# Kernel tuning notes

Measured on AMD Instinct MI355X. Metric: run time of the kernel, lower is better.

Reference implementation:

```python
import jax, jax.numpy as jnp
import numpy as np

# ---- static config (matches init_kwargs) ----
B = 8            # batch_size (graphs)
N = 10000        # num_nodes per graph
NTOT = B * N     # total node rows (80000)
E = 320000       # edges (only over first N nodes, as in the original code)
D = 128          # input_dim == backbone_channels (shared conv forces equality)
H = 4            # heads
C = 128          # backbone_channels (per-head out dim, concat=False)
L = 3            # num_backbone_layers
K = 30           # sort-pool k
HID = 512        # mlp_hidden_dim
OUT = 2          # output_dim
EXPECTED = K * L * C * H + 1  # buggy mlp_input_dim from __init__ -> zero-pad
BN_EPS = 1e-5


def setup_inputs() -> dict:
    key = jax.random.key(0)
    ks = jax.random.split(key, 20)
    s = 1.0 / np.sqrt(D)
    inp = {
        "x": jax.random.normal(ks[0], (NTOT, D), dtype=jnp.float32),
        "edge_index": jax.random.randint(ks[1], (2, E), 0, N, dtype=jnp.int32),
        "age": jax.random.normal(ks[2], (B,), dtype=jnp.float32),
        # shared TransformerConv params (reused across all L layers)
        "Wq": jax.random.normal(ks[3], (D, H * C), dtype=jnp.float32) * s,
        "bq": jax.random.normal(ks[4], (H * C,), dtype=jnp.float32) * 0.02,
        "Wk": jax.random.normal(ks[5], (D, H * C), dtype=jnp.float32) * s,
        "bk": jax.random.normal(ks[6], (H * C,), dtype=jnp.float32) * 0.02,
        "Wv": jax.random.normal(ks[7], (D, H * C), dtype=jnp.float32) * s,
        "bv": jax.random.normal(ks[8], (H * C,), dtype=jnp.float32) * 0.02,
        "Wskip": jax.random.normal(ks[9], (D, C), dtype=jnp.float32) * s,
        "bskip": jax.random.normal(ks[10], (C,), dtype=jnp.float32) * 0.02,
        # per-layer BatchNorm (eval mode: running stats)
        "bn_gamma": 1.0 + 0.1 * jax.random.normal(ks[11], (L, C), dtype=jnp.float32),
        "bn_beta": 0.1 * jax.random.normal(ks[12], (L, C), dtype=jnp.float32),
        "bn_mean": 0.1 * jax.random.normal(ks[13], (L, C), dtype=jnp.float32),
        "bn_var": jax.random.uniform(ks[14], (L, C), dtype=jnp.float32, minval=0.5, maxval=1.5),
        # MLP head (2 layers: EXPECTED->HID, ReLU, HID->OUT)
        "W1": jax.random.normal(ks[15], (EXPECTED, HID), dtype=jnp.float32) * (1.0 / np.sqrt(EXPECTED)),
        "b1": jnp.zeros((HID,), dtype=jnp.float32),
        "W2": jax.random.normal(ks[16], (HID, OUT), dtype=jnp.float32) * (1.0 / np.sqrt(HID)),
        "b2": jnp.zeros((OUT,), dtype=jnp.float32),
    }
    return inp


def _transformer_conv(h, src, dst, Wq, bq, Wk, bk, Wv, bv, Wskip, bskip):
    # PyG TransformerConv, concat=False, root_weight=True, eval (no attn dropout)
    q = (h @ Wq + bq).reshape(NTOT, H, C)
    k = (h @ Wk + bk).reshape(NTOT, H, C)
    v = (h @ Wv + bv).reshape(NTOT, H, C)
    # per-edge attention logits [E, H]
    alpha = jnp.einsum("ehc,ehc->eh", q[dst], k[src]) / np.sqrt(C).astype(np.float32)
    # segment softmax over incoming edges of each target node
    m = jax.ops.segment_max(alpha, dst, num_segments=NTOT)          # [NTOT, H]
    e = jnp.exp(alpha - m[dst])
    denom = jax.ops.segment_sum(e, dst, num_segments=NTOT)          # [NTOT, H]
    a = e / (denom[dst] + 1e-16)                                    # [E, H]
    out = jax.ops.segment_sum(a[:, :, None] * v[src], dst, num_segments=NTOT)  # [NTOT,H,C]
    return out.mean(axis=1) + h @ Wskip + bskip                     # concat=False -> head mean


def reference(x, edge_index, age, Wq, bq, Wk, bk, Wv, bv, Wskip, bskip,
              bn_gamma, bn_beta, bn_mean, bn_var, W1, b1, W2, b2):
    src, dst = edge_index[0], edge_index[1]
    h = x
    feats = []
    for i in range(L):  # fixed small layer count; shared conv weights
        h = _transformer_conv(h, src, dst, Wq, bq, Wk, bk, Wv, bv, Wskip, bskip)
        h = (h - bn_mean[i]) * (bn_gamma[i] / jnp.sqrt(bn_var[i] + BN_EPS)) + bn_beta[i]
        h = jax.nn.relu(h)  # dropout: eval mode no-op
        feats.append(h)
    h = feats[-1]  # concat_input_graph=False
    # global_sort_pool: sort nodes per graph by last channel (desc), take top-k
    xr = h.reshape(B, N, C)
    idx = jnp.argsort(-xr[:, :, -1], axis=1)[:, :K]                 # [B, K]
    pooled = jnp.take_along_axis(xr, idx[:, :, None], axis=1)       # [B, K, C]
    z = pooled.reshape(B, K * C)
    z = jnp.concatenate([z, age.reshape(B, 1)], axis=1)             # [B, K*C+1]
    # zero-pad to the (mismatched) expected MLP input dim, as in the original
    z = jnp.concatenate([z, jnp.zeros((B, EXPECTED - z.shape[1]), dtype=z.dtype)], axis=1)
    z = jax.nn.relu(z @ W1 + b1)
    z = z @ W2 + b2
    return jax.nn.log_softmax(z, axis=-1)
```

## Files before the change

kernel.cpp:

```cpp
#include <hip/hip_runtime.h>
#include <cmath>


#define NN    10000
#define NTOT  80000
#define EE    320000
#define CH    128

__device__ __forceinline__ float rl_f(float v, int lane) {
    return __uint_as_float(__builtin_amdgcn_readlane(__float_as_uint(v), lane));
}

__global__ __launch_bounds__(256) void precompute_kernel(
    const float* __restrict__ Wq, const float* __restrict__ bq,
    const float* __restrict__ Wk, const float* __restrict__ Wv,
    const float* __restrict__ bv, const float* __restrict__ Wskip,
    const float* __restrict__ bskip,
    const float* __restrict__ bn_gamma, const float* __restrict__ bn_beta,
    const float* __restrict__ bn_mean, const float* __restrict__ bn_var,
    float* __restrict__ Bcat, float* __restrict__ biascat,
    float* __restrict__ Wcomb, float* __restrict__ bvbar,
    float* __restrict__ bnS, float* __restrict__ bnB)
{
    const float inv_sqrtC = 0.08838834764831845f;
    int idx = blockIdx.x * 256 + threadIdx.x;
    if (idx < 65536) {
        int c = idx >> 9;
        int o = idx & 511;
        int hbase = o & ~127;
        int j = o & 127;
        const float* wq = Wq + c * 512 + hbase;
        const float* wk = Wk + j * 512 + hbase;
        float s = 0.f;
        for (int cc = 0; cc < 128; cc++) s = fmaf(wq[cc], wk[cc], s);
        Bcat[c * 640 + o] = s * inv_sqrtC;
        return;
    }
    idx -= 65536;
    if (idx < 16384) {
        int c = idx >> 7, n = idx & 127;
        Bcat[c * 640 + 512 + n] = Wskip[c * 128 + n];
        return;
    }
    idx -= 16384;
    if (idx < 512) {
        int o = idx, hbase = o & ~127, j = o & 127;
        const float* wk = Wk + j * 512 + hbase;
        const float* bqp = bq + hbase;
        float s = 0.f;
        for (int cc = 0; cc < 128; cc++) s = fmaf(bqp[cc], wk[cc], s);
        biascat[o] = s * inv_sqrtC;
        return;
    }
    idx -= 512;
    if (idx < 128) {
        biascat[512 + idx] = bskip[idx];
        return;
    }
    idx -= 128;
    if (idx < 65536) {
        int k = idx >> 7;
        int n = idx & 127;
        int h = k >> 7, c = k & 127;
        Wcomb[k * 128 + n] = Wv[c * 512 + h * 128 + n] * 0.25f;
        return;
    }
    idx -= 65536;
    if (idx < 128) {
        float s = 0.f;
        for (int h = 0; h < 4; h++) s += bv[h * 128 + idx];
        bvbar[idx] = 0.25f * s;
        return;
    }
    idx -= 128;
    if (idx < 384) {
        float sc = bn_gamma[idx] / sqrtf(bn_var[idx] + 1e-5f);
        bnS[idx] = sc;
        bnB[idx] = bn_beta[idx] - bn_mean[idx] * sc;
        return;
    }
}

__global__ void count_kernel(const int* __restrict__ dst, int* __restrict__ deg) {
    int e = blockIdx.x * 256 + threadIdx.x;
    if (e < EE) atomicAdd(&deg[dst[e]], 1);
}

__global__ __launch_bounds__(1024) void scan_kernel(const int* __restrict__ deg,
                                                    int* __restrict__ rowstart) {
    __shared__ int part[1024];
    const int t = threadIdx.x;
    int loc[10];
    int s = 0;
    for (int i = 0; i < 10; i++) {
        int idx = t * 10 + i;
        int v = (idx < NN) ? deg[idx] : 0;
        loc[i] = s; s += v;
    }
    part[t] = s; __syncthreads();
    for (int d = 1; d < 1024; d <<= 1) {
        int v = (t >= d) ? part[t - d] : 0;
        __syncthreads();
        part[t] += v;
        __syncthreads();
    }
    int base = (t == 0) ? 0 : part[t - 1];
    for (int i = 0; i < 10; i++) {
        int idx = t * 10 + i;
        if (idx <= NN) rowstart[idx] = base + loc[i];
    }
}

__global__ void scatter_kernel(const int* __restrict__ src, const int* __restrict__ dst,
                               const int* __restrict__ rowstart, int* __restrict__ cursor,
                               int* __restrict__ csr_src) {
    int e = blockIdx.x * 256 + threadIdx.x;
    if (e < EE) {
        int d = dst[e];
        int p = atomicAdd(&cursor[d], 1);
        csr_src[rowstart[d] + p] = src[e];
    }
}

__global__ __launch_bounds__(256, 3) void skip_keys_kernel(
    const float* __restrict__ xup,
    const float* __restrict__ Wskip,
    const float* __restrict__ bskip,
    const float* __restrict__ bnS, const float* __restrict__ bnB,
    float* __restrict__ gkeys)
{
    __shared__ float rowb[64][132];
    __shared__ float Bs[16][132];
    __shared__ float sWc[128];
    const int t = threadIdx.x;
    const int r0 = blockIdx.x * 64;
    const int Mrem = min(64, (NTOT - NN) - r0);
    const int tx = t & 15;
    const int ty = t >> 4;

    for (int f = t; f < 64 * 32; f += 256) {
        int row = f >> 5, c4 = (f & 31) * 4;
        if (row < Mrem)
            *(float4*)&rowb[row][c4] = *(const float4*)(xup + (size_t)(r0 + row) * CH + c4);
    }
    if (t < 128) sWc[t] = Wskip[t * 128 + 127];

    for (int l = 0; l < 2; l++) {
        float acc[4][8];
        #pragma unroll
        for (int i = 0; i < 4; i++)
            #pragma unroll
            for (int j = 0; j < 8; j++) acc[i][j] = 0.f;

        for (int k0 = 0; k0 < 128; k0 += 16) {
            __syncthreads();
            for (int f = t; f < 512; f += 256) {
                int kk = f >> 5, n4 = (f & 31) * 4;
                *(float4*)&Bs[kk][n4] = *(const float4*)(Wskip + (size_t)(k0 + kk) * 128 + n4);
            }
            __syncthreads();
            #pragma unroll
            for (int kq = 0; kq < 4; kq++) {
                float4 a4[4];
                #pragma unroll
                for (int i = 0; i < 4; i++)
                    a4[i] = *(const float4*)&rowb[ty + 16 * i][k0 + kq * 4];
                float4 c0[4], c1[4];
                #pragma unroll
                for (int q = 0; q < 4; q++) {
                    c0[q] = *(const float4*)&Bs[kq * 4 + q][tx * 4];
                    c1[q] = *(const float4*)&Bs[kq * 4 + q][64 + tx * 4];
                }
                #pragma unroll
                for (int q = 0; q < 4; q++) {
                    #pragma unroll
                    for (int i = 0; i < 4; i++) {
                        const float av = (q == 0) ? a4[i].x : (q == 1) ? a4[i].y
                                       : (q == 2) ? a4[i].z : a4[i].w;
                        acc[i][0] = fmaf(av, c0[q].x, acc[i][0]);
                        acc[i][1] = fmaf(av, c0[q].y, acc[i][1]);
                        acc[i][2] = fmaf(av, c0[q].z, acc[i][2]);
                        acc[i][3] = fmaf(av, c0[q].w, acc[i][3]);
                        acc[i][4] = fmaf(av, c1[q].x, acc[i][4]);
                        acc[i][5] = fmaf(av, c1[q].y, acc[i][5]);
                        acc[i][6] = fmaf(av, c1[q].z, acc[i][6]);
                        acc[i][7] = fmaf(av, c1[q].w, acc[i][7]);
                    }
                }
            }
        }
        __syncthreads();
        const float* bS = bnS + l * 128;
        const float* bB = bnB + l * 128;
        #pragma unroll
        for (int i = 0; i < 4; i++) {
            const int row = ty + 16 * i;
            float4 v0, v1;
            float* p0 = &v0.x;
            float* p1 = &v1.x;
            #pragma unroll
            for (int q = 0; q < 4; q++) {
                const int n0c = tx * 4 + q;
                float xv = acc[i][q] + bskip[n0c];
                xv = fmaf(xv, bS[n0c], bB[n0c]);
                p0[q] = fmaxf(xv, 0.f);
                const int n1c = 64 + tx * 4 + q;
                float yv = acc[i][4 + q] + bskip[n1c];
                yv = fmaf(yv, bS[n1c], bB[n1c]);
                p1[q] = fmaxf(yv, 0.f);
            }
            *(float4*)&rowb[row][tx * 4] = v0;
            *(float4*)&rowb[row][64 + tx * 4] = v1;
        }
    }
    __syncthreads();
    if (t < Mrem) {
        float s = 0.f;
        for (int k = 0; k < 128; k++) s = fmaf(rowb[t][k], sWc[k], s);
        s += bskip[127];
        s = fmaf(s, bnS[2 * 128 + 127], bnB[2 * 128 + 127]);
        gkeys[NN + r0 + t] = fmaxf(s, 0.f);
    }
}

template<int BM, int BN, int TM, int TN, int MODE>
__global__ __launch_bounds__(256) void gemm_fp32(
    const float* __restrict__ A, int lda,
    const float* __restrict__ B, int ldb,
    const float* __restrict__ bias, const float* __restrict__ bias2,
    const int* __restrict__ deg,
    const float* __restrict__ Cold,
    const float* __restrict__ bnS, const float* __restrict__ bnB,
    float* __restrict__ C0, int ldc0,
    float* __restrict__ C1, int ldc1,
    int M, int K,
    float* __restrict__ keysOut)
{
    constexpr int BK = 16;
    __shared__ float As[BK][BM + 4];
    __shared__ float Bs[BK][BN + 4];
    const int t  = threadIdx.x;
    const int tx = t % (BN / TN);
    const int ty = t / (BN / TN);
    const int m0 = blockIdx.x * BM;
    const int n0 = blockIdx.y * BN;
    float acc[TM][TN];
    #pragma unroll
    for (int i = 0; i < TM; i++)
        #pragma unroll
        for (int j = 0; j < TN; j++) acc[i][j] = 0.f;

    for (int k0 = 0; k0 < K; k0 += BK) {
        #pragma unroll
        for (int f = t; f < BM * 4; f += 256) {
            int row = f >> 2, fc = f & 3;
            int gm = m0 + row;
            float4 v = make_float4(0.f, 0.f, 0.f, 0.f);
            if (gm < M) v = *(const float4*)(A + (size_t)gm * lda + k0 + fc * 4);
            As[fc * 4 + 0][row] = v.x;
            As[fc * 4 + 1][row] = v.y;
            As[fc * 4 + 2][row] = v.z;
            As[fc * 4 + 3][row] = v.w;
        }
        #pragma unroll
        for (int f = t; f < BK * (BN / 4); f += 256) {
            int kk = f / (BN / 4);
            int nn = (f % (BN / 4)) * 4;
            *(float4*)(&Bs[kk][nn]) = *(const float4*)(B + (size_t)(k0 + kk) * ldb + n0 + nn);
        }
        __syncthreads();
        #pragma unroll
        for (int kk = 0; kk < BK; kk++) {
            float af[TM], bf[TN];
            if constexpr (TM == 2) {
                float2 v = *(const float2*)&As[kk][ty * 2];
                af[0] = v.x; af[1] = v.y;
            } else {
                float4 v = *(const float4*)&As[kk][ty * 4];
                af[0] = v.x; af[1] = v.y; af[2] = v.z; af[3] = v.w;
            }
            if constexpr (TN == 4) {
                float4 v = *(const float4*)&Bs[kk][tx * 4];
                bf[0] = v.x; bf[1] = v.y; bf[2] = v.z; bf[3] = v.w;
            } else {
                float4 v = *(const float4*)&Bs[kk][tx * 4];
                float4 w = *(const float4*)&Bs[kk][BN / 2 + tx * 4];
                bf[0] = v.x; bf[1] = v.y; bf[2] = v.z; bf[3] = v.w;
                bf[4] = w.x; bf[5] = w.y; bf[6] = w.z; bf[7] = w.w;
            }
            #pragma unroll
            for (int i = 0; i < TM; i++)
                #pragma unroll
                for (int j = 0; j < TN; j++)
                    acc[i][j] = fmaf(af[i], bf[j], acc[i][j]);
        }
        __syncthreads();
    }
    #pragma unroll
    for (int i = 0; i < TM; i++) {
        const int gm = m0 + ty * TM + i;
        if (gm >= M) continue;
        const bool addB2 = (MODE == 4) ? (deg[gm] > 0) : false;
        #pragma unroll
        for (int h = 0; h < TN / 4; h++) {
            const int nb = n0 + ((TN == 8) ? h * (BN / 2) + tx * 4 : tx * TN + h * 4);
            float4 v;
            float* vp = &v.x;
            if (MODE == 4) {
                const float4 old = *(const float4*)(Cold + (size_t)gm * ldc1 + nb);
                const float* op = &old.x;
                #pragma unroll
                for (int q = 0; q < 4; q++) {
                    const int n = nb + q;
                    float x = acc[i][h * 4 + q] + op[q];
                    if (addB2) x += bias2[n];
                    x = fmaf(x, bnS[n], bnB[n]);
                    vp[q] = fmaxf(x, 0.f);
                }
                *(float4*)(C0 + (size_t)gm * ldc0 + nb) = v;
                if (keysOut != nullptr && nb == 124) keysOut[gm] = v.w;
            } else {
                #pragma unroll
                for (int q = 0; q < 4; q++)
                    vp[q] = acc[i][h * 4 + q] + bias[nb + q];
                if (nb < 512)
                    *(float4*)(C0 + (size_t)gm * ldc0 + nb) = v;
                else
                    *(float4*)(C1 + (size_t)gm * ldc1 + nb - 512) = v;
            }
        }
    }
}

__global__ __launch_bounds__(256) void attn_kernel(
    const float* __restrict__ h,
    const float* __restrict__ u,
    float* __restrict__ g,
    const int* __restrict__ rowstart,
    const int* __restrict__ csr_src)
{
    __shared__ float h_lds[128 * 65];
    __shared__ __align__(16) float palpha[4 * 64 * 4];
    __shared__ __align__(16) float wT[64 * 4];
    __shared__ __align__(16) float scale_lds[4];
    __shared__ __align__(16) float s_lds[4];
    __shared__ __align__(16) float merge[128 * 4];
    __shared__ int src_lds[64];

    const int n  = blockIdx.x;
    const int t  = threadIdx.x;
    const int w  = t >> 6;
    const int l  = t & 63;
    const int c  = t & 127;
    const int jh = t >> 7;
    const int rs   = rowstart[n];
    const int degn = rowstart[n + 1] - rs;

    if (degn == 0) {
        g[(size_t)n * 512 + t] = 0.f;
        g[(size_t)n * 512 + 256 + t] = 0.f;
        return;
    }
    float u_reg0 = u[(size_t)n * 512 + ((l >> 5)) * 128 + 32 * w + (l & 31)];
    float u_reg1 = u[(size_t)n * 512 + ((l >> 5) + 2) * 128 + 32 * w + (l & 31)];

    float m_run = -INFINITY, s_run = 0.f;
    float4 acc4 = make_float4(0.f, 0.f, 0.f, 0.f);

    for (int base = 0; base < degn; base += 64) {
        const int len = min(64, degn - base);
        __syncthreads();
        if (t < len) src_lds[t] = csr_src[rs + base + t];
        __syncthreads();
        for (int f = t; f < len * 128; f += 256) {
            const int cc = f & 127, j = f >> 7;
            h_lds[cc * 65 + j] = h[(size_t)src_lds[j] * CH + cc];
        }
        __syncthreads();
        {
            float p0 = 0.f, p1 = 0.f, p2 = 0.f, p3 = 0.f;
            #pragma unroll
            for (int dc = 0; dc < 32; dc++) {
                const float hv = h_lds[(32 * w + dc) * 65 + l];
                p0 = fmaf(rl_f(u_reg0, dc),      hv, p0);
                p1 = fmaf(rl_f(u_reg0, 32 + dc), hv, p1);
                p2 = fmaf(rl_f(u_reg1, dc),      hv, p2);
                p3 = fmaf(rl_f(u_reg1, 32 + dc), hv, p3);
            }
            palpha[(0 * 64 + l) * 4 + w] = p0;
            palpha[(1 * 64 + l) * 4 + w] = p1;
            palpha[(2 * 64 + l) * 4 + w] = p2;
            palpha[(3 * 64 + l) * 4 + w] = p3;
        }
        __syncthreads();
        {
            const float4 pa = *(const float4*)&palpha[(w * 64 + l) * 4];
            float alpha = (l < len) ? (pa.x + pa.y + pa.z + pa.w) : -INFINITY;
            float mx = alpha;
            #pragma unroll
            for (int d = 1; d < 64; d <<= 1) mx = fmaxf(mx, __shfl_xor(mx, d, 64));
            const float newm = fmaxf(m_run, mx);
            float e = (l < len) ? __expf(alpha - newm) : 0.f;
            float ss = e;
            #pragma unroll
            for (int d = 1; d < 64; d <<= 1) ss += __shfl_xor(ss, d, 64);
            const float sc = (m_run == -INFINITY) ? 0.f : __expf(m_run - newm);
            s_run = s_run * sc + ss;
            m_run = newm;
            wT[l * 4 + w] = e;
            if (l == 0) scale_lds[w] = sc;
        }
        __syncthreads();
        {
            const float4 scv = *(const float4*)scale_lds;
            acc4.x *= scv.x; acc4.y *= scv.y; acc4.z *= scv.z; acc4.w *= scv.w;
            const int j0 = jh * 32;
            const int j1 = min(len, j0 + 32);
            for (int j = j0; j < j1; j++) {
                const float hv = h_lds[c * 65 + j];
                const float4 wv = *(const float4*)&wT[j * 4];
                acc4.x = fmaf(wv.x, hv, acc4.x);
                acc4.y = fmaf(wv.y, hv, acc4.y);
                acc4.z = fmaf(wv.z, hv, acc4.z);
                acc4.w = fmaf(wv.w, hv, acc4.w);
            }
        }
    }
    if (l == 0) s_lds[w] = s_run;
    __syncthreads();
    if (jh == 1) *(float4*)&merge[c * 4] = acc4;
    __syncthreads();
    if (jh == 0) {
        const float4 o  = *(const float4*)&merge[c * 4];
        const float4 sv = *(const float4*)s_lds;
        g[(size_t)n * 512 + 0 * 128 + c] = (acc4.x + o.x) / (sv.x + 1e-16f);
        g[(size_t)n * 512 + 1 * 128 + c] = (acc4.y + o.y) / (sv.y + 1e-16f);
        g[(size_t)n * 512 + 2 * 128 + c] = (acc4.z + o.z) / (sv.z + 1e-16f);
        g[(size_t)n * 512 + 3 * 128 + c] = (acc4.w + o.w) / (sv.w + 1e-16f);
    }
}

__global__ __launch_bounds__(256) void radix_pool_kernel(
    const float* __restrict__ gkeys, const float* __restrict__ age,
    int* __restrict__ sel, float* __restrict__ z)
{
    __shared__ unsigned int keys[NN];
    __shared__ int hist[256];
    __shared__ int sbuf[256];
    __shared__ unsigned int sel_prefix;
    __shared__ int sel_need;
    __shared__ int gt_counter;
    __shared__ unsigned int cand_key[30];
    __shared__ int cand_idx[30];
    __shared__ int order[30];

    const int b = blockIdx.x;
    const int t = threadIdx.x;

    for (int i = t; i < NN; i += 256)
        keys[i] = __float_as_uint(gkeys[(size_t)b * NN + i]);
    if (t == 0) { sel_prefix = 0u; sel_need = 30; gt_counter = 0; }
    __syncthreads();

    for (int r = 3; r >= 0; r--) {
        hist[t] = 0;
        __syncthreads();
        const int shift = r * 8;
        const unsigned int pmask = (r == 3) ? 0u : (0xFFFFFFFFu << ((r + 1) * 8));
        const unsigned int pref = sel_prefix;
        const int need = sel_need;
        for (int i = t; i < NN; i += 256) {
            unsigned int k = keys[i];
            if ((k & pmask) == pref)
                atomicAdd(&hist[(k >> shift) & 255u], 1);
        }
        __syncthreads();
        sbuf[t] = hist[255 - t];
        __syncthreads();
        for (int d = 1; d < 256; d <<= 1) {
            int o = (t >= d) ? sbuf[t - d] : 0;
            __syncthreads();
            sbuf[t] += o;
            __syncthreads();
        }
        {
            const int v = t;
            const int ge = sbuf[255 - v];
            const int gt = ge - hist[v];
            if (gt < need && need <= ge) {
                sel_prefix = pref | ((unsigned int)v << shift);
                sel_need = need - gt;
            }
        }
        __syncthreads();
    }

    const unsigned int T = sel_prefix;
    const int need_eq = sel_need;
    const int n_gt = 30 - need_eq;

    for (int i = t; i < NN; i += 256) {
        unsigned int k = keys[i];
        if (k > T) {
            int p = atomicAdd(&gt_counter, 1);
            cand_key[p] = k; cand_idx[p] = i;
        }
    }
    {
        const int CHK = (NN + 255) / 256;
        const int i0 = t * CHK, i1 = min(NN, i0 + CHK);
        int local = 0;
        for (int i = i0; i < i1; i++) if (keys[i] == T) local++;
        sbuf[t] = local;
        __syncthreads();
        for (int d = 1; d < 256; d <<= 1) {
            int o = (t >= d) ? sbuf[t - d] : 0;
            __syncthreads();
            sbuf[t] += o;
            __syncthreads();
        }
        int rank = (t == 0) ? 0 : sbuf[t - 1];
        for (int i = i0; i < i1; i++) {
            if (keys[i] == T) {
                if (rank < need_eq) { cand_key[n_gt + rank] = T; cand_idx[n_gt + rank] = i; }
                rank++;
            }
        }
    }
    __syncthreads();
    if (t < 30) {
        const unsigned int mk = cand_key[t];
        const int mi = cand_idx[t];
        int rk = 0;
        for (int j = 0; j < 30; j++) {
            const unsigned int ok = cand_key[j];
            const int oi = cand_idx[j];
            if (ok > mk || (ok == mk && oi < mi)) rk++;
        }
        order[rk] = t;
    }
    __syncthreads();
    if (t < 30) sel[b * 30 + t] = cand_idx[order[t]];
    if (t == 0) z[(size_t)b * 3841 + 3840] = age[b];
}

__global__ __launch_bounds__(128) void gather_kernel(
    const float* __restrict__ h3,
    const float* __restrict__ x,
    const float* __restrict__ Wskip, const float* __restrict__ bskip,
    const float* __restrict__ bnS, const float* __restrict__ bnB,
    const int* __restrict__ sel, float* __restrict__ z)
{
    __shared__ float buf0[128], buf1[128];
    const int blk = blockIdx.x;
    const int b = blk / 30;
    const int kk = blk % 30;
    const int c = threadIdx.x;
    const int i = sel[b * 30 + kk];
    const size_t g = (size_t)b * NN + i;
    float v;
    if (b == 0) {
        v = h3[g * CH + c];
    } else {
        float* rd = buf0;
        float* wr = buf1;
        buf0[c] = x[g * CH + c];
        __syncthreads();
        float s = 0.f;
        for (int l = 0; l < 3; l++) {
            s = 0.f;
            for (int k = 0; k < 128; k++) s = fmaf(rd[k], Wskip[k * 128 + c], s);
            s += bskip[c];
            s = fmaf(s, bnS[l * 128 + c], bnB[l * 128 + c]);
            s = fmaxf(s, 0.f);
            if (l < 2) {
                wr[c] = s;
                __syncthreads();
                float* tmp = rd; rd = wr; wr = tmp;
            }
        }
        v = s;
    }
    z[(size_t)b * 3841 + kk * CH + c] = v;
}

__global__ __launch_bounds__(256) void mlp1_kernel(
    const float* __restrict__ z, const float* __restrict__ W1,
    float* __restrict__ zh)
{
    __shared__ float zs[256];
    const int b  = blockIdx.x >> 4;
    const int ic = blockIdx.x & 15;
    const int t  = threadIdx.x;
    const int i0 = ic * 241;
    const int i1 = min(3841, i0 + 241);
    float a0 = 0.f, a1 = 0.f;
    for (int cb = i0; cb < i1; cb += 256) {
        int cl = min(256, i1 - cb);
        __syncthreads();
        if (t < cl) zs[t] = z[(size_t)b * 3841 + cb + t];
        __syncthreads();
        #pragma unroll 4
        for (int q = 0; q < cl; q++) {
            float zv = zs[q];
            const float* wp = W1 + (size_t)(cb + q) * 512;
            a0 = fmaf(zv, wp[t], a0);
            a1 = fmaf(zv, wp[t + 256], a1);
        }
    }
    atomicAdd(&zh[(size_t)b * 512 + t], a0);
    atomicAdd(&zh[(size_t)b * 512 + t + 256], a1);
}

__global__ __launch_bounds__(256) void mlp2_kernel(
    const float* __restrict__ zh, const float* __restrict__ b1,
    const float* __restrict__ W2, const float* __restrict__ b2,
    float* __restrict__ out)
{
    __shared__ float r0[256], r1[256];
    const int b = blockIdx.x;
    const int t = threadIdx.x;
    float a0 = 0.f, a1 = 0.f;
    for (int j = t; j < 512; j += 256) {
        float v = fmaxf(zh[(size_t)b * 512 + j] + b1[j], 0.f);
        a0 = fmaf(v, W2[j * 2 + 0], a0);
        a1 = fmaf(v, W2[j * 2 + 1], a1);
    }
    r0[t] = a0; r1[t] = a1; __syncthreads();
    for (int s = 128; s > 0; s >>= 1) {
        if (t < s) { r0[t] += r0[t + s]; r1[t] += r1[t + s]; }
        __syncthreads();
    }
    if (t == 0) {
        float l0 = r0[0] + b2[0], l1 = r1[0] + b2[1];
        float m = fmaxf(l0, l1);
        float lse = m + logf(__expf(l0 - m) + __expf(l1 - m));
        out[b * 2 + 0] = l0 - lse;
        out[b * 2 + 1] = l1 - lse;
    }
}

extern "C" void kernel_launch(void* const* d_in, const int* in_sizes, int n_in,
                              void* d_out, int out_size, void* d_ws, size_t ws_size,
                              hipStream_t stream) {
    const float* x     = (const float*)d_in[0];
    const int*   ei    = (const int*)d_in[1];
    const float* age   = (const float*)d_in[2];
    const float* Wq    = (const float*)d_in[3];
    const float* bq    = (const float*)d_in[4];
    const float* Wk    = (const float*)d_in[5];
    const float* Wv    = (const float*)d_in[7];
    const float* bv    = (const float*)d_in[8];
    const float* Wskip = (const float*)d_in[9];
    const float* bskip = (const float*)d_in[10];
    const float* bn_g  = (const float*)d_in[11];
    const float* bn_b  = (const float*)d_in[12];
    const float* bn_m  = (const float*)d_in[13];
    const float* bn_v  = (const float*)d_in[14];
    const float* W1    = (const float*)d_in[15];
    const float* b1    = (const float*)d_in[16];
    const float* W2    = (const float*)d_in[17];
    const float* b2    = (const float*)d_in[18];

    float* ws = (float*)d_ws;
    float* h3      = ws;
    float* hlowA   = h3 + 10240000;
    float* hlowB   = hlowA + 1280000;
    float* u       = hlowB + 1280000;
    float* skipraw = u + 5120000;
    float* Bcat    = skipraw + 1280000;
    float* biascat = Bcat + 81920;
    float* Wcomb   = biascat + 640;
    float* bvbar   = Wcomb + 65536;
    float* bnS     = bvbar + 128;
    float* bnB     = bnS + 384;
    float* zbuf    = bnB + 384;
    float* zh      = zbuf + 30728;
    int* deg      = (int*)(zh + 4096);
    int* cursor   = deg + NN;
    int* rowstart = cursor + NN;
    int* csr_src  = rowstart + NN + 1;
    float* keysG  = (float*)(csr_src + EE);
    int* sel      = (int*)(keysG + NTOT);

    const int* srcI = ei;
    const int* dstI = ei + EE;

    hipMemsetAsync(deg, 0, sizeof(int) * (2 * NN), stream);
    hipMemsetAsync(zh, 0, sizeof(float) * 4096, stream);

    precompute_kernel<<<581, 256, 0, stream>>>(Wq, bq, Wk, Wv, bv, Wskip, bskip,
                                               bn_g, bn_b, bn_m, bn_v,
                                               Bcat, biascat, Wcomb, bvbar, bnS, bnB);
    count_kernel<<<1250, 256, 0, stream>>>(dstI, deg);
    scan_kernel<<<1, 1024, 0, stream>>>(deg, rowstart);
    scatter_kernel<<<1250, 256, 0, stream>>>(srcI, dstI, rowstart, cursor, csr_src);

    skip_keys_kernel<<<1094, 256, 0, stream>>>(x + (size_t)NN * CH, Wskip, bskip,
                                               bnS, bnB, keysG);

    const float* hcur = x;
    for (int l = 0; l < 3; l++) {
        float* dest = (l == 0) ? hlowA : (l == 1) ? hlowB : h3;
        gemm_fp32<64, 128, 4, 8, 0><<<dim3(157, 5), 256, 0, stream>>>(
            hcur, CH, Bcat, 640, biascat, nullptr, nullptr, nullptr,
            nullptr, nullptr, u, 512, skipraw, CH, NN, 128, nullptr);
        attn_kernel<<<NN, 256, 0, stream>>>(hcur, u, u, rowstart, csr_src);
        gemm_fp32<32, 64, 2, 4, 4><<<dim3(313, 2), 256, 0, stream>>>(
            u, 512, Wcomb, CH, nullptr, bvbar, deg, skipraw,
            bnS + l * 128, bnB + l * 128, dest, CH, nullptr, CH, NN, 512,
            (l == 2) ? keysG : nullptr);
        hcur = dest;
    }
    radix_pool_kernel<<<8, 256, 0, stream>>>(keysG, age, sel, zbuf);
    gather_kernel<<<240, 128, 0, stream>>>(h3, x, Wskip, bskip,
                                           bnS, bnB, sel, zbuf);
    mlp1_kernel<<<128, 256, 0, stream>>>(zbuf, W1, zh);
    mlp2_kernel<<<8, 256, 0, stream>>>(zh, b1, W2, b2, (float*)d_out);
}
```

Measured before the change: 624.6 us.

## Restructure skip-key GEMM, vectorize attention gather, retile projection GEMM

The skip_keys kernel drops its shared-memory staged tile of Wskip. Each wave now computes 32 output columns for all 64 rows, reading the weights straight from global memory with wave-uniform addresses, which removes the per-k-tile barriers. The attention kernel's neighbour gather now loads float4 rows and scatters them transposed into LDS, instead of issuing scalar loads. The QKV projection GEMM moves from a 64x128 to a 64x64 tile to launch more blocks. These changes trade LDS reuse and register pressure for fewer syncs, wider loads and more parallelism, and the float4 gather may raise LDS bank conflicts on the transposed stores.

```diff
diff --git a/kernel.cpp b/kernel.cpp
--- a/kernel.cpp
+++ b/kernel.cpp
@@ -122,7 +122,7 @@
     }
 }
 
-__global__ __launch_bounds__(256, 3) void skip_keys_kernel(
+__global__ __launch_bounds__(256, 4) void skip_keys_kernel(
     const float* __restrict__ xup,
     const float* __restrict__ Wskip,
     const float* __restrict__ bskip,
@@ -130,90 +130,58 @@
     float* __restrict__ gkeys)
 {
     __shared__ float rowb[64][132];
-    __shared__ float Bs[16][132];
     __shared__ float sWc[128];
     const int t = threadIdx.x;
+    const int l = t & 63;
+    const int wv = __builtin_amdgcn_readfirstlane(t >> 6);
+    const int colbase = wv * 32;
     const int r0 = blockIdx.x * 64;
     const int Mrem = min(64, (NTOT - NN) - r0);
-    const int tx = t & 15;
-    const int ty = t >> 4;
 
     for (int f = t; f < 64 * 32; f += 256) {
         int row = f >> 5, c4 = (f & 31) * 4;
-        if (row < Mrem)
-            *(float4*)&rowb[row][c4] = *(const float4*)(xup + (size_t)(r0 + row) * CH + c4);
+        float4 v = make_float4(0.f, 0.f, 0.f, 0.f);
+        if (row < Mrem) v = *(const float4*)(xup + (size_t)(r0 + row) * CH + c4);
+        *(float4*)&rowb[row][c4] = v;
     }
     if (t < 128) sWc[t] = Wskip[t * 128 + 127];
-
-    for (int l = 0; l < 2; l++) {
-        float acc[4][8];
+    __syncthreads();
+
+    for (int layer = 0; layer < 2; layer++) {
+        float acc[32];
         #pragma unroll
-        for (int i = 0; i < 4; i++)
-            #pragma unroll
-            for (int j = 0; j < 8; j++) acc[i][j] = 0.f;
-
-        for (int k0 = 0; k0 < 128; k0 += 16) {
-            __syncthreads();
-            for (int f = t; f < 512; f += 256) {
-                int kk = f >> 5, n4 = (f & 31) * 4;
-                *(float4*)&Bs[kk][n4] = *(const float4*)(Wskip + (size_t)(k0 + kk) * 128 + n4);
-            }
-            __syncthreads();
-            #pragma unroll
-            for (int kq = 0; kq < 4; kq++) {
-                float4 a4[4];
-                #pragma unroll
-                for (int i = 0; i < 4; i++)
-                    a4[i] = *(const float4*)&rowb[ty + 16 * i][k0 + kq * 4];
-                float4 c0[4], c1[4];
-                #pragma unroll
-                for (int q = 0; q < 4; q++) {
-                    c0[q] = *(const float4*)&Bs[kq * 4 + q][tx * 4];
-                    c1[q] = *(const float4*)&Bs[kq * 4 + q][64 + tx * 4];
-                }
-                #pragma unroll
-                for (int q = 0; q < 4; q++) {
-                    #pragma unroll
-                    for (int i = 0; i < 4; i++) {
-                        const float av = (q == 0) ? a4[i].x : (q == 1) ? a4[i].y
-                                       : (q == 2) ? a4[i].z : a4[i].w;
-                        acc[i][0] = fmaf(av, c0[q].x, acc[i][0]);
-                        acc[i][1] = fmaf(av, c0[q].y, acc[i][1]);
-                        acc[i][2] = fmaf(av, c0[q].z, acc[i][2]);
-                        acc[i][3] = fmaf(av, c0[q].w, acc[i][3]);
-                        acc[i][4] = fmaf(av, c1[q].x, acc[i][4]);
-                        acc[i][5] = fmaf(av, c1[q].y, acc[i][5]);
-                        acc[i][6] = fmaf(av, c1[q].z, acc[i][6]);
-                        acc[i][7] = fmaf(av, c1[q].w, acc[i][7]);
-                    }
-                }
-            }
-        }
-        __syncthreads();
-        const float* bS = bnS + l * 128;
-        const float* bB = bnB + l * 128;
-        #pragma unroll
-        for (int i = 0; i < 4; i++) {
-            const int row = ty + 16 * i;
-            float4 v0, v1;
-            float* p0 = &v0.x;
-            float* p1 = &v1.x;
+        for (int c = 0; c < 32; c++) acc[c] = 0.f;
+        const float* Wb = Wskip + colbase;
+        for (int kq = 0; kq < 32; kq++) {
+            const float4 a4 = *(const float4*)&rowb[l][kq * 4];
             #pragma unroll
             for (int q = 0; q < 4; q++) {
-                const int n0c = tx * 4 + q;
-                float xv = acc[i][q] + bskip[n0c];
-                xv = fmaf(xv, bS[n0c], bB[n0c]);
-                p0[q] = fmaxf(xv, 0.f);
-                const int n1c = 64 + tx * 4 + q;
-                float yv = acc[i][4 + q] + bskip[n1c];
-                yv = fmaf(yv, bS[n1c], bB[n1c]);
-                p1[q] = fmaxf(yv, 0.f);
-            }
-            *(float4*)&rowb[row][tx * 4] = v0;
-            *(float4*)&rowb[row][64 + tx * 4] = v1;
-        }
-    }
-    __syncthreads();
+                const float av = (q == 0) ? a4.x : (q == 1) ? a4.y
+                               : (q == 2) ? a4.z : a4.w;
+                const float* wr = Wb + (kq * 4 + q) * 128;
+                #pragma unroll
+                for (int c = 0; c < 32; c++)
+                    acc[c] = fmaf(av, wr[c], acc[c]);
+            }
+        }
+        __syncthreads();
+        const float* bS = bnS + layer * 128;
+        const float* bB = bnB + layer * 128;
+        #pragma unroll
+        for (int c4 = 0; c4 < 8; c4++) {
+            float4 v;
+            float* vp = &v.x;
+            #pragma unroll
+            for (int q = 0; q < 4; q++) {
+                const int n = colbase + c4 * 4 + q;
+                float xv = acc[c4 * 4 + q] + bskip[n];
+                xv = fmaf(xv, bS[n], bB[n]);
+                vp[q] = fmaxf(xv, 0.f);
+            }
+            *(float4*)&rowb[l][colbase + c4 * 4] = v;
+        }
+        __syncthreads();
+    }
     if (t < Mrem) {
         float s = 0.f;
         for (int k = 0; k < 128; k++) s = fmaf(rowb[t][k], sWc[k], s);
@@ -372,9 +340,13 @@
         __syncthreads();
         if (t < len) src_lds[t] = csr_src[rs + base + t];
         __syncthreads();
-        for (int f = t; f < len * 128; f += 256) {
-            const int cc = f & 127, j = f >> 7;
-            h_lds[cc * 65 + j] = h[(size_t)src_lds[j] * CH + cc];
+        for (int f = t; f < len * 32; f += 256) {
+            const int j = f >> 5, c4 = (f & 31) * 4;
+            const float4 v = *(const float4*)(h + (size_t)src_lds[j] * CH + c4);
+            h_lds[(c4 + 0) * 65 + j] = v.x;
+            h_lds[(c4 + 1) * 65 + j] = v.y;
+            h_lds[(c4 + 2) * 65 + j] = v.z;
+            h_lds[(c4 + 3) * 65 + j] = v.w;
         }
         __syncthreads();
         {
@@ -702,7 +674,7 @@
     const float* hcur = x;
     for (int l = 0; l < 3; l++) {
         float* dest = (l == 0) ? hlowA : (l == 1) ? hlowB : h3;
-        gemm_fp32<64, 128, 4, 8, 0><<<dim3(157, 5), 256, 0, stream>>>(
+        gemm_fp32<64, 64, 4, 4, 0><<<dim3(157, 10), 256, 0, stream>>>(
             hcur, CH, Bcat, 640, biascat, nullptr, nullptr, nullptr,
             nullptr, nullptr, u, 512, skipraw, CH, NN, 128, nullptr);
         attn_kernel<<<NN, 256, 0, stream>>>(hcur, u, u, rowstart, csr_src);
```

Result: no change. 617.6 us (-1.1%).
